# Kernel tuning notes

Hardware: AMD Instinct MI355X
Metric: run time of the kernel (lower is better)

## Reference

```python
import jax, jax.numpy as jnp
import numpy as np

N = 50000        # nodes
E = 400000       # edges (no self-loops; self-loops appended in forward)
IN_DIM = 128
H, C = 4, 64     # heads, channels per head
D = H * C        # 256
NEG_SLOPE = 0.2


def setup_inputs() -> dict:
    key = jax.random.key(0)
    ks = jax.random.split(key, 8)
    x = jax.random.normal(ks[0], (N, IN_DIM), jnp.float32)
    # build edges with no self-loops (src != dst), matching the module's mask
    src = jax.random.randint(ks[1], (E,), 0, N)
    off = jax.random.randint(ks[2], (E,), 1, N)
    dst = (src + off) % N
    edge_index = jnp.stack([src, dst]).astype(jnp.int32)
    inp = {"x": x, "edge_index": edge_index}
    dims_in = [IN_DIM, D, D, D, D]
    for l in range(5):
        k = jax.random.split(ks[3 + l], 4)
        inp[f"W{l}"] = jax.random.normal(k[0], (D, dims_in[l]), jnp.float32) * 0.05
        inp[f"att_src{l}"] = jax.random.normal(k[1], (1, H, C), jnp.float32) * 0.05
        inp[f"att_dst{l}"] = jax.random.normal(k[2], (1, H, C), jnp.float32) * 0.05
        inp[f"bias{l}"] = jnp.zeros((D,), jnp.float32)
    return inp


def _gat_layer(x, W, a_src, a_dst, b, src, dst, relu_out):
    # linear projection, reshape to [N, H, C]
    h = (x @ W.T).reshape(N, H, C)
    alpha_src = jnp.sum(h * a_src, axis=-1)   # [N, H]
    alpha_dst = jnp.sum(h * a_dst, axis=-1)   # [N, H]
    # per-edge logits: alpha_j (source) + alpha_i (dest)
    alpha = jax.nn.leaky_relu(alpha_src[src] + alpha_dst[dst], negative_slope=NEG_SLOPE)  # [E', H]
    # segment softmax over destination neighborhoods (max is detached, as in the original)
    m = jax.lax.stop_gradient(jax.ops.segment_max(alpha, dst, num_segments=N))  # [N, H]
    e = jnp.exp(alpha - m[dst])
    s = jax.ops.segment_sum(e, dst, num_segments=N) + 1e-16
    a = e / s[dst]                                                             # [E', H]
    # weighted scatter-add aggregation of gathered source features
    out = jax.ops.segment_sum(a[:, :, None] * h[src], dst, num_segments=N)     # [N, H, C]
    out = out.reshape(N, D) + b
    return jax.nn.relu(out) if relu_out else out


def reference(x, edge_index,
              W0, att_src0, att_dst0, bias0,
              W1, att_src1, att_dst1, bias1,
              W2, att_src2, att_dst2, bias2,
              W3, att_src3, att_dst3, bias3,
              W4, att_src4, att_dst4, bias4):
    # input edges contain no self-loops; append one self-loop per node (as in the trace)
    loops = jnp.arange(N, dtype=edge_index.dtype)
    src = jnp.concatenate([edge_index[0], loops])
    dst = jnp.concatenate([edge_index[1], loops])
    params = [(W0, att_src0, att_dst0, bias0), (W1, att_src1, att_dst1, bias1),
              (W2, att_src2, att_dst2, bias2), (W3, att_src3, att_dst3, bias3),
              (W4, att_src4, att_dst4, bias4)]
    h = x
    for l, (W, a_s, a_d, b) in enumerate(params):
        h = _gat_layer(h, W, a_s, a_d, b, src, dst, relu_out=(l < 4))
    return h
```

## Files before the change

### kernel.cpp

```cpp
#include <hip/hip_runtime.h>
#include <hip/hip_bf16.h>

#define H 4
#define D 256
#define NEG_SLOPE 0.2f

typedef __attribute__((ext_vector_type(8))) _Float16 f16x8;
typedef __attribute__((ext_vector_type(4))) _Float16 f16x4;
typedef __attribute__((ext_vector_type(4))) float f32x4;

__global__ void k_cvt(const float* __restrict__ in, _Float16* __restrict__ out, int n4) {
    int i = blockIdx.x * blockDim.x + threadIdx.x;
    if (i >= n4) return;
    float4 v = ((const float4*)in)[i];
    f16x4 o = {(_Float16)v.x, (_Float16)v.y, (_Float16)v.z, (_Float16)v.w};
    *(f16x4*)&out[(size_t)i * 4] = o;
}

template<int K>
__device__ __forceinline__ void cvt_wfrag_one(const float* __restrict__ W,
                                              _Float16* __restrict__ wfrag, int idx) {
    const int NKS = K / 32;
    if (idx >= 16 * NKS * 64) return;
    int l  = idx & 63;
    int ks = (idx >> 6) % NKS;
    int c16 = idx / (NKS * 64);
    int col = c16 * 16 + (l & 15);
    int k0  = ks * 32 + (l >> 4) * 8;
    const float* src = &W[(size_t)col * K + k0];
    float4 v0 = *(const float4*)src;
    float4 v1 = *(const float4*)(src + 4);
    f16x8 o = {(_Float16)v0.x, (_Float16)v0.y, (_Float16)v0.z, (_Float16)v0.w,
               (_Float16)v1.x, (_Float16)v1.y, (_Float16)v1.z, (_Float16)v1.w};
    *(f16x8*)&wfrag[(size_t)idx * 8] = o;
}

__global__ void k_cvt_wfrag0(const float* __restrict__ W, _Float16* __restrict__ wfrag) {
    cvt_wfrag_one<128>(W, wfrag, blockIdx.x * blockDim.x + threadIdx.x);
}

__global__ void k_cvt_wfrag_all(const float* __restrict__ w1, const float* __restrict__ w2,
                                const float* __restrict__ w3, const float* __restrict__ w4,
                                _Float16* __restrict__ wfrag) {
    const float* ws[4] = {w1, w2, w3, w4};
    int l = blockIdx.y;
    cvt_wfrag_one<256>(ws[l], wfrag + 128 * 256 + (size_t)l * 256 * 256,
                       blockIdx.x * blockDim.x + threadIdx.x);
}

template<int K>
__global__ __launch_bounds__(256) void k_gemm_mfma(
        const _Float16* __restrict__ xf, const _Float16* __restrict__ wfrag,
        const float* __restrict__ att_src, const float* __restrict__ att_dst,
        _Float16* __restrict__ hmat, float* __restrict__ alpha_src,
        float* __restrict__ alpha_dst, int nrows) {
    const int NKS = K / 32;
    __shared__ _Float16 sw[8 * NKS * 64 * 8];
    int t = threadIdx.x;
    int w = t >> 6, l = t & 63;
    int r = l & 15, q = l >> 4;
    int row0  = blockIdx.x * 64;
    int split = blockIdx.y;

    {
        const uint4* wsrc = (const uint4*)(wfrag + (size_t)split * 8 * NKS * 64 * 8);
        uint4* wdst = (uint4*)sw;
        const int nchunk = 8 * NKS * 64;
        #pragma unroll
        for (int i = 0; i < nchunk / 256; ++i)
            wdst[i * 256 + t] = wsrc[i * 256 + t];
    }

    int gr_a = row0 + w * 16 + r;
    bool aok = (gr_a < nrows);
    f16x8 a[NKS];
    #pragma unroll
    for (int ks = 0; ks < NKS; ++ks) {
        if (aok) a[ks] = *(const f16x8*)&xf[(size_t)gr_a * K + ks * 32 + q * 8];
        else     a[ks] = (f16x8){0, 0, 0, 0, 0, 0, 0, 0};
    }

    __syncthreads();

    f32x4 acc[8];
    #pragma unroll
    for (int cf = 0; cf < 8; ++cf) acc[cf] = (f32x4){0.f, 0.f, 0.f, 0.f};
    #pragma unroll
    for (int cf = 0; cf < 8; ++cf) {
        f16x8 b[NKS];
        #pragma unroll
        for (int ks = 0; ks < NKS; ++ks)
            b[ks] = *(f16x8*)&sw[(size_t)((cf * NKS + ks) * 64 + l) * 8];
        #pragma unroll
        for (int ks = 0; ks < NKS; ++ks)
            acc[cf] = __builtin_amdgcn_mfma_f32_16x16x32_f16(a[ks], b[ks], acc[cf], 0, 0, 0);
    }

    #pragma unroll
    for (int cf = 0; cf < 8; ++cf) {
        #pragma unroll
        for (int i = 0; i < 4; ++i) {
            int gr = row0 + w * 16 + q * 4 + i;
            if (gr < nrows)
                hmat[(size_t)gr * D + split * 128 + cf * 16 + r] = (_Float16)acc[cf][i];
        }
    }
    float asv[8], adv[8];
    #pragma unroll
    for (int cf = 0; cf < 8; ++cf) {
        asv[cf] = att_src[split * 128 + cf * 16 + r];
        adv[cf] = att_dst[split * 128 + cf * 16 + r];
    }
    #pragma unroll
    for (int i = 0; i < 4; ++i) {
        #pragma unroll
        for (int hh = 0; hh < 2; ++hh) {
            float ps = 0.f, pd = 0.f;
            #pragma unroll
            for (int j = 0; j < 4; ++j) {
                int cf = hh * 4 + j;
                ps += acc[cf][i] * asv[cf];
                pd += acc[cf][i] * adv[cf];
            }
            #pragma unroll
            for (int m = 1; m < 16; m <<= 1) {
                ps += __shfl_xor(ps, m);
                pd += __shfl_xor(pd, m);
            }
            int gr = row0 + w * 16 + q * 4 + i;
            if (r == 0 && gr < nrows) {
                alpha_src[gr * 4 + split * 2 + hh] = ps;
                alpha_dst[gr * 4 + split * 2 + hh] = pd;
            }
        }
    }
}

__global__ void k_deg(const int* __restrict__ ei, int E, int E2, int* __restrict__ deg) {
    int e = blockIdx.x * blockDim.x + threadIdx.x;
    if (e >= E2) return;
    int de = (e < E) ? ei[E + e] : (e - E);
    atomicAdd(&deg[de], 1);
}

__global__ void k_scan_block(const int* __restrict__ deg, int* __restrict__ incl,
                             int* __restrict__ bsum, int n) {
    __shared__ int sd[256];
    int t = threadIdx.x;
    int i = blockIdx.x * 256 + t;
    int v = (i < n) ? deg[i] : 0;
    sd[t] = v;
    __syncthreads();
    for (int off = 1; off < 256; off <<= 1) {
        int add = (t >= off) ? sd[t - off] : 0;
        __syncthreads();
        sd[t] += add;
        __syncthreads();
    }
    if (i < n) incl[i] = sd[t];
    if (t == 255) bsum[blockIdx.x] = sd[255];
}

__global__ void k_scan_bsum(int* __restrict__ bsum, int nb) {
    __shared__ int sd[256];
    int t = threadIdx.x;
    int v = (t < nb) ? bsum[t] : 0;
    sd[t] = v;
    __syncthreads();
    for (int off = 1; off < 256; off <<= 1) {
        int add = (t >= off) ? sd[t - off] : 0;
        __syncthreads();
        sd[t] += add;
        __syncthreads();
    }
    if (t < nb) bsum[t] = sd[t] - v;
}

__global__ void k_rowptr(const int* __restrict__ incl, const int* __restrict__ deg,
                         const int* __restrict__ boff, int* __restrict__ row_ptr,
                         int n, int total) {
    int i = blockIdx.x * blockDim.x + threadIdx.x;
    if (i < n) row_ptr[i] = incl[i] - deg[i] + boff[i >> 8];
    if (i == 0) row_ptr[n] = total;
}

__global__ void k_scatter(const int* __restrict__ ei, int E, int E2,
                          const int* __restrict__ row_ptr, int* __restrict__ cursor,
                          int* __restrict__ csr_src) {
    int e = blockIdx.x * blockDim.x + threadIdx.x;
    if (e >= E2) return;
    int se, de;
    if (e < E) { se = ei[e]; de = ei[E + e]; }
    else       { se = e - E; de = se; }
    int pos = atomicAdd(&cursor[de], 1);
    csr_src[row_ptr[de] + pos] = se;
}

__global__ __launch_bounds__(256) void k_aggregate(const _Float16* __restrict__ hmat,
        const int* __restrict__ row_ptr, const int* __restrict__ csr_src,
        const float* __restrict__ alpha_src, const float* __restrict__ alpha_dst,
        const float* __restrict__ bias, float* __restrict__ outf,
        _Float16* __restrict__ outx, int relu, int nrows) {
    int wid  = (blockIdx.x * 256 + threadIdx.x) >> 6;
    int lane = threadIdx.x & 63;
    int node = wid * 2 + (lane >> 5);
    if (node >= nrows) return;
    int c    = lane & 31;
    int head = c >> 3;
    int st = row_ptr[node], en = row_ptr[node + 1];
    int deg = en - st;
    float a_d = alpha_dst[node * 4 + head];
    float acc[8] = {};
    float ssum = 0.f;
    for (int b = 0; b < deg; b += 8) {
        int sn[8];
        #pragma unroll
        for (int j = 0; j < 8; ++j) {
            int e = b + j;
            int li = st + (e < deg ? e : deg - 1);
            sn[j] = csr_src[li];
        }
        f16x8 hv[8];
        #pragma unroll
        for (int j = 0; j < 8; ++j)
            hv[j] = *(const f16x8*)&hmat[(size_t)sn[j] * D + c * 8];
        float as[8];
        #pragma unroll
        for (int j = 0; j < 8; ++j) as[j] = alpha_src[sn[j] * 4 + head];
        #pragma unroll
        for (int j = 0; j < 8; ++j) {
            float a = as[j] + a_d;
            a = a > 0.f ? a : NEG_SLOPE * a;
            float ex = (b + j < deg) ? __expf(a) : 0.f;
            ssum += ex;
            #pragma unroll
            for (int k = 0; k < 8; ++k) acc[k] += ex * (float)hv[j][k];
        }
    }
    float sinv = 1.f / (ssum + 1e-16f);
    float4 b0 = *(const float4*)&bias[c * 8];
    float4 b1 = *(const float4*)&bias[c * 8 + 4];
    float o[8];
    o[0] = acc[0] * sinv + b0.x; o[1] = acc[1] * sinv + b0.y;
    o[2] = acc[2] * sinv + b0.z; o[3] = acc[3] * sinv + b0.w;
    o[4] = acc[4] * sinv + b1.x; o[5] = acc[5] * sinv + b1.y;
    o[6] = acc[6] * sinv + b1.z; o[7] = acc[7] * sinv + b1.w;
    if (relu) {
        #pragma unroll
        for (int k = 0; k < 8; ++k) o[k] = fmaxf(o[k], 0.f);
    }
    if (outx) {
        f16x8 o8 = {(_Float16)o[0], (_Float16)o[1], (_Float16)o[2], (_Float16)o[3],
                    (_Float16)o[4], (_Float16)o[5], (_Float16)o[6], (_Float16)o[7]};
        *(f16x8*)&outx[(size_t)node * D + c * 8] = o8;
    } else {
        *(float4*)&outf[(size_t)node * D + c * 8] =
            make_float4(o[0], o[1], o[2], o[3]);
        *(float4*)&outf[(size_t)node * D + c * 8 + 4] =
            make_float4(o[4], o[5], o[6], o[7]);
    }
}

extern "C" void kernel_launch(void* const* d_in, const int* in_sizes, int n_in,
                              void* d_out, int out_size, void* d_ws, size_t ws_size,
                              hipStream_t stream) {
    const float* x = (const float*)d_in[0];
    const int* ei = (const int*)d_in[1];
    const int N  = in_sizes[0] / 128;
    const int E  = in_sizes[1] / 2;
    const int E2 = E + N;

    char* wsp = (char*)d_ws;
    size_t off = 0;
    auto alloc = [&](size_t bytes) -> void* {
        void* p = wsp + off;
        off += (bytes + 255) & ~(size_t)255;
        return p;
    };
    _Float16* bufH  = (_Float16*)alloc((size_t)N * D * 2);
    _Float16* xf16  = (_Float16*)alloc((size_t)N * D * 2);
    _Float16* wfrag = (_Float16*)alloc((size_t)(128 * 256 + 4 * 256 * 256) * 2);
    float* alpha_src = (float*)alloc((size_t)N * H * 4);
    float* alpha_dst = (float*)alloc((size_t)N * H * 4);
    int*   deg       = (int*)alloc((size_t)N * 4);
    int*   incl      = (int*)alloc((size_t)N * 4);
    int*   bsum      = (int*)alloc(256 * 4);
    int*   row_ptr   = (int*)alloc((size_t)(N + 1) * 4);
    int*   cursor    = (int*)alloc((size_t)N * 4);
    int*   csr_src   = (int*)alloc((size_t)E2 * 4);
    (void)ws_size;

    hipMemsetAsync(deg, 0, (size_t)N * 4, stream);
    hipMemsetAsync(cursor, 0, (size_t)N * 4, stream);

    int nx4 = N * 128 / 4;
    k_cvt<<<(nx4 + 255) / 256, 256, 0, stream>>>(x, xf16, nx4);
    k_cvt_wfrag0<<<(16 * 4 * 64 + 255) / 256, 256, 0, stream>>>(
        (const float*)d_in[2], wfrag);
    dim3 wg((16 * 8 * 64 + 255) / 256, 4);
    k_cvt_wfrag_all<<<wg, 256, 0, stream>>>(
        (const float*)d_in[6], (const float*)d_in[10],
        (const float*)d_in[14], (const float*)d_in[18], wfrag);

    int egrid = (E2 + 255) / 256;
    k_deg<<<egrid, 256, 0, stream>>>(ei, E, E2, deg);
    int nb = (N + 255) / 256;
    k_scan_block<<<nb, 256, 0, stream>>>(deg, incl, bsum, N);
    k_scan_bsum<<<1, 256, 0, stream>>>(bsum, nb);
    k_rowptr<<<nb, 256, 0, stream>>>(incl, deg, bsum, row_ptr, N, E2);
    k_scatter<<<egrid, 256, 0, stream>>>(ei, E, E2, row_ptr, cursor, csr_src);

    dim3 ggrid((N + 63) / 64, 2);
    int agrid = (N + 7) / 8;
    for (int l = 0; l < 5; ++l) {
        const float* as_ = (const float*)d_in[3 + 4 * l];
        const float* ad_ = (const float*)d_in[4 + 4 * l];
        const float* bs_ = (const float*)d_in[5 + 4 * l];
        const _Float16* wl = (l == 0) ? wfrag
                           : wfrag + 128 * 256 + (size_t)(l - 1) * 256 * 256;

        if (l == 0)
            k_gemm_mfma<128><<<ggrid, 256, 0, stream>>>(xf16, wl, as_, ad_,
                                                        bufH, alpha_src, alpha_dst, N);
        else
            k_gemm_mfma<256><<<ggrid, 256, 0, stream>>>(xf16, wl, as_, ad_,
                                                        bufH, alpha_src, alpha_dst, N);

        int last = (l == 4);
        k_aggregate<<<agrid, 256, 0, stream>>>(bufH, row_ptr, csr_src,
                                               alpha_src, alpha_dst, bs_,
                                               last ? (float*)d_out : nullptr,
                                               last ? nullptr : xf16,
                                               last ? 0 : 1, N);
    }
}
```

Measured before the change: 402.6 us.

## Fuse input fp32-to-fp16 conversion into first GEMM, prefetch CSR indices in aggregate

The first-layer GEMM now reads fp32 x directly and converts it to fp16 in registers, so the separate conversion kernel and its round trip through memory are gone. The GEMM grid is flattened to 1D with the two column halves of each row tile in adjacent blocks, which may improve L2 reuse of the A rows. The aggregation loop now software-prefetches the next batch of 8 source indices while the current batch is processed, hiding the dependent index-load latency at the cost of a few more registers.

```diff
diff --git a/kernel.cpp b/kernel.cpp
--- a/kernel.cpp
+++ b/kernel.cpp
@@ -8,14 +8,6 @@
 typedef __attribute__((ext_vector_type(8))) _Float16 f16x8;
 typedef __attribute__((ext_vector_type(4))) _Float16 f16x4;
 typedef __attribute__((ext_vector_type(4))) float f32x4;
-
-__global__ void k_cvt(const float* __restrict__ in, _Float16* __restrict__ out, int n4) {
-    int i = blockIdx.x * blockDim.x + threadIdx.x;
-    if (i >= n4) return;
-    float4 v = ((const float4*)in)[i];
-    f16x4 o = {(_Float16)v.x, (_Float16)v.y, (_Float16)v.z, (_Float16)v.w};
-    *(f16x4*)&out[(size_t)i * 4] = o;
-}
 
 template<int K>
 __device__ __forceinline__ void cvt_wfrag_one(const float* __restrict__ W,
@@ -48,9 +40,9 @@
                        blockIdx.x * blockDim.x + threadIdx.x);
 }
 
-template<int K>
+template<int K, bool F32X>
 __global__ __launch_bounds__(256) void k_gemm_mfma(
-        const _Float16* __restrict__ xf, const _Float16* __restrict__ wfrag,
+        const void* __restrict__ xin, const _Float16* __restrict__ wfrag,
         const float* __restrict__ att_src, const float* __restrict__ att_dst,
         _Float16* __restrict__ hmat, float* __restrict__ alpha_src,
         float* __restrict__ alpha_dst, int nrows) {
@@ -59,8 +51,8 @@
     int t = threadIdx.x;
     int w = t >> 6, l = t & 63;
     int r = l & 15, q = l >> 4;
-    int row0  = blockIdx.x * 64;
-    int split = blockIdx.y;
+    int row0  = (blockIdx.x >> 1) * 64;
+    int split = blockIdx.x & 1;
 
     {
         const uint4* wsrc = (const uint4*)(wfrag + (size_t)split * 8 * NKS * 64 * 8);
@@ -76,8 +68,20 @@
     f16x8 a[NKS];
     #pragma unroll
     for (int ks = 0; ks < NKS; ++ks) {
-        if (aok) a[ks] = *(const f16x8*)&xf[(size_t)gr_a * K + ks * 32 + q * 8];
-        else     a[ks] = (f16x8){0, 0, 0, 0, 0, 0, 0, 0};
+        if (aok) {
+            if constexpr (F32X) {
+                const float* xs = (const float*)xin + (size_t)gr_a * K + ks * 32 + q * 8;
+                float4 v0 = *(const float4*)xs;
+                float4 v1 = *(const float4*)(xs + 4);
+                a[ks] = (f16x8){(_Float16)v0.x, (_Float16)v0.y, (_Float16)v0.z,
+                                (_Float16)v0.w, (_Float16)v1.x, (_Float16)v1.y,
+                                (_Float16)v1.z, (_Float16)v1.w};
+            } else {
+                a[ks] = *(const f16x8*)((const _Float16*)xin + (size_t)gr_a * K + ks * 32 + q * 8);
+            }
+        } else {
+            a[ks] = (f16x8){0, 0, 0, 0, 0, 0, 0, 0};
+        }
     }
 
     __syncthreads();
@@ -209,17 +213,17 @@
     int head = c >> 3;
     int st = row_ptr[node], en = row_ptr[node + 1];
     int deg = en - st;
+    int nbatch = (deg + 7) >> 3;
     float a_d = alpha_dst[node * 4 + head];
     float acc[8] = {};
     float ssum = 0.f;
-    for (int b = 0; b < deg; b += 8) {
-        int sn[8];
-        #pragma unroll
-        for (int j = 0; j < 8; ++j) {
-            int e = b + j;
-            int li = st + (e < deg ? e : deg - 1);
-            sn[j] = csr_src[li];
-        }
+    int sn[8];
+    #pragma unroll
+    for (int j = 0; j < 8; ++j) {
+        int li = st + (j < deg ? j : deg - 1);
+        sn[j] = csr_src[li];
+    }
+    for (int b = 0; b < nbatch; ++b) {
         f16x8 hv[8];
         #pragma unroll
         for (int j = 0; j < 8; ++j)
@@ -227,15 +231,26 @@
         float as[8];
         #pragma unroll
         for (int j = 0; j < 8; ++j) as[j] = alpha_src[sn[j] * 4 + head];
+        int sn2[8];
+        if (b + 1 < nbatch) {
+            #pragma unroll
+            for (int j = 0; j < 8; ++j) {
+                int e = (b + 1) * 8 + j;
+                int li = st + (e < deg ? e : deg - 1);
+                sn2[j] = csr_src[li];
+            }
+        }
         #pragma unroll
         for (int j = 0; j < 8; ++j) {
             float a = as[j] + a_d;
             a = a > 0.f ? a : NEG_SLOPE * a;
-            float ex = (b + j < deg) ? __expf(a) : 0.f;
+            float ex = (b * 8 + j < deg) ? __expf(a) : 0.f;
             ssum += ex;
             #pragma unroll
             for (int k = 0; k < 8; ++k) acc[k] += ex * (float)hv[j][k];
         }
+        #pragma unroll
+        for (int j = 0; j < 8; ++j) sn[j] = sn2[j];
     }
     float sinv = 1.f / (ssum + 1e-16f);
     float4 b0 = *(const float4*)&bias[c * 8];
@@ -293,8 +308,6 @@
     hipMemsetAsync(deg, 0, (size_t)N * 4, stream);
     hipMemsetAsync(cursor, 0, (size_t)N * 4, stream);
 
-    int nx4 = N * 128 / 4;
-    k_cvt<<<(nx4 + 255) / 256, 256, 0, stream>>>(x, xf16, nx4);
     k_cvt_wfrag0<<<(16 * 4 * 64 + 255) / 256, 256, 0, stream>>>(
         (const float*)d_in[2], wfrag);
     dim3 wg((16 * 8 * 64 + 255) / 256, 4);
@@ -310,7 +323,7 @@
     k_rowptr<<<nb, 256, 0, stream>>>(incl, deg, bsum, row_ptr, N, E2);
     k_scatter<<<egrid, 256, 0, stream>>>(ei, E, E2, row_ptr, cursor, csr_src);
 
-    dim3 ggrid((N + 63) / 64, 2);
+    int ggrid = ((N + 63) / 64) * 2;
     int agrid = (N + 7) / 8;
     for (int l = 0; l < 5; ++l) {
         const float* as_ = (const float*)d_in[3 + 4 * l];
@@ -320,10 +333,10 @@
                            : wfrag + 128 * 256 + (size_t)(l - 1) * 256 * 256;
 
         if (l == 0)
-            k_gemm_mfma<128><<<ggrid, 256, 0, stream>>>(xf16, wl, as_, ad_,
+            k_gemm_mfma<128, true><<<ggrid, 256, 0, stream>>>(x, wl, as_, ad_,
                                                         bufH, alpha_src, alpha_dst, N);
         else
-            k_gemm_mfma<256><<<ggrid, 256, 0, stream>>>(xf16, wl, as_, ad_,
+            k_gemm_mfma<256, false><<<ggrid, 256, 0, stream>>>(xf16, wl, as_, ad_,
                                                         bufH, alpha_src, alpha_dst, N);
 
         int last = (l == 4);
```

Result: faster. 392.3 us (-2.6%).
